# Kernel optimization log

Measured on AMD Instinct MI355X. Metric: run time of the kernel, lower is better.

The kernel has to match this reference:

```python
import jax, jax.numpy as jnp
import numpy as np

N_E = 1024
E_DIM = 256
BETA = 0.25
B, L = 32, 1024


def setup_inputs() -> dict:
    key = jax.random.key(0)
    k1, k2 = jax.random.split(key)
    z = jax.random.normal(k1, (B, E_DIM, L), dtype=jnp.float32)
    mask = jnp.ones((B, L), dtype=jnp.float32)
    embedding = jax.random.uniform(k2, (N_E, E_DIM), dtype=jnp.float32,
                                   minval=-1.0 / N_E, maxval=1.0 / N_E)
    return {"z": z, "mask": mask, "embedding": embedding}


def reference(z, mask, embedding):
    # conv branch: (B, C, L) -> (B, L, C) -> (N, C)
    Bz, C, Lz = z.shape
    zp = jnp.transpose(z, (0, 2, 1))          # (B, L, C)
    zf = zp.reshape(-1, C)                    # (N, C)

    # squared L2 distance to every codebook entry: ||z||^2 + ||e||^2 - 2 z.e
    d = (jnp.sum(zf * zf, axis=1, keepdims=True)
         + jnp.sum(embedding * embedding, axis=1)
         - 2.0 * (zf @ embedding.T))          # (N, n_e)
    idx = jnp.argmin(d, axis=1)               # (N,)

    # gather == one_hot @ embedding
    z_q = embedding[idx].reshape(Bz, Lz, C)   # (B, L, C)

    m = mask[..., None]                       # (B, L, 1)
    commitment_loss = jnp.mean(((jax.lax.stop_gradient(z_q) - zp) * m) ** 2)
    codebook_loss = jnp.mean(((z_q - jax.lax.stop_gradient(zp)) * m) ** 2)
    loss = commitment_loss + BETA * codebook_loss

    # straight-through estimator
    z_q_st = zp + jax.lax.stop_gradient(z_q - zp)

    one_hot = jax.nn.one_hot(idx, N_E, dtype=zf.dtype)           # (N, n_e)
    e_mean = jnp.zeros((N_E,), zf.dtype).at[idx].add(1.0) / idx.shape[0]
    perplexity = jnp.exp(-jnp.sum(e_mean * jnp.log(e_mean + 1e-10)))

    z_q_out = jnp.transpose(z_q_st, (0, 2, 1))  # back to (B, C, L)
    return (loss, z_q_out, perplexity, one_hot, idx[:, None])
```

## Files before the change

### kernel.cpp

```cpp
#include <hip/hip_runtime.h>

constexpr int B_ = 32, C_ = 256, L_ = 1024, NE = 1024;
constexpr int NPTS = B_ * L_;
constexpr long long LOSS_OFF = 0;
constexpr long long ZQ_OFF   = 1;
constexpr long long PERP_OFF = 1 + 8388608;
constexpr long long OH_OFF   = PERP_OFF + 1;
constexpr long long IDX_OFF  = OH_OFF + 33554432LL;
constexpr size_t WS_IDX = 0;
constexpr size_t WS_CNT = 131072;
constexpr size_t WS_LP  = 135168;
constexpr size_t WS_E2  = 139264;

constexpr float MARGIN = 7e-4f;

typedef _Float16 f16x8 __attribute__((ext_vector_type(8)));
typedef float    f32x4 __attribute__((ext_vector_type(4)));

__device__ inline unsigned fkey(float f) {
  unsigned u = __float_as_uint(f);
  return (u & 0x80000000u) ? ~u : (u | 0x80000000u);
}
__device__ inline float unfkey(unsigned k) {
  unsigned u = (k & 0x80000000u) ? (k ^ 0x80000000u) : ~k;
  return __uint_as_float(u);
}

__global__ __launch_bounds__(256) void k_prep_ehl(const float* __restrict__ emb,
                                                  uint4* __restrict__ ehlF) {
  const int u = blockIdx.x * 256 + threadIdx.x;
  const int c16 = u & 15;
  const int s8  = (u >> 4) & 31;
  const int g   = u >> 9;
  const int code = g * 16 + c16;
  const float4* e4 = reinterpret_cast<const float4*>(emb + (size_t)code * C_) + s8 * 2;
  float4 v0 = e4[0], v1 = e4[1];
  const float f[8] = {v0.x, v0.y, v0.z, v0.w, v1.x, v1.y, v1.z, v1.w};
  unsigned w[4];
#pragma unroll
  for (int i = 0; i < 4; ++i) {
    _Float16 h0 = (_Float16)f[2 * i];
    _Float16 h1 = (_Float16)f[2 * i + 1];
    w[i] = (unsigned)__builtin_bit_cast(unsigned short, h0) |
           ((unsigned)__builtin_bit_cast(unsigned short, h1) << 16);
  }
  ehlF[u] = make_uint4(w[0], w[1], w[2], w[3]);
}

__global__ __launch_bounds__(64) void k_prep_e2(const float* __restrict__ emb,
                                                float* __restrict__ e2,
                                                unsigned* __restrict__ counts) {
  const int j = blockIdx.x;
  const int t = threadIdx.x;
  const float* row = emb + (size_t)j * C_;
  double s = 0.0;
#pragma unroll
  for (int q = 0; q < 4; ++q) {
    float v = row[t + 64 * q];
    s += (double)v * (double)v;
  }
#pragma unroll
  for (int off = 32; off > 0; off >>= 1) s += __shfl_down(s, off);
  if (t == 0) { e2[j] = (float)s; counts[j] = 0u; }
}

__global__ __launch_bounds__(512, 1) void k_screen_rr(const float* __restrict__ z,
                                                      const float* __restrict__ emb,
                                                      const uint4* __restrict__ ehlF,
                                                      const float* __restrict__ e2g,
                                                      int* __restrict__ idxw,
                                                      unsigned* __restrict__ counts,
                                                      float* __restrict__ idx_out) {
  __shared__ _Float16 Az[128 * 256];
  __shared__ double zpart[128][17];
  __shared__ unsigned short cand[128 * 32];
  __shared__ unsigned long long bestkey[128];
  __shared__ unsigned minkey[128];
  __shared__ unsigned ccnt[128];
  __shared__ float z2s[128];
  __shared__ int ids[128];
  __shared__ unsigned char dcnt[128];
  __shared__ float zcol[256];
  __shared__ int nbad;

  const int tid  = threadIdx.x;
  const int lane = tid & 63;
  const int wid  = tid >> 6;
  const int wr   = wid >> 2;
  const int wc   = wid & 3;
  const int l15  = lane & 15;
  const int lhi  = lane >> 4;
  const int n0   = blockIdx.x * 128;
  const int b    = blockIdx.x >> 3;
  const int l0   = (blockIdx.x & 7) << 7;

  {
    const float4* z4 = reinterpret_cast<const float4*>(z + (size_t)b * (C_ * L_) + l0);
    const int l4 = tid & 31;
    const int kp = tid >> 5;
    double sj[4] = {0.0, 0.0, 0.0, 0.0};
#pragma unroll
    for (int rr = 0; rr < 8; ++rr) {
      const int k0 = rr * 32 + kp * 2;
      float4 a0 = z4[(size_t)k0 * (L_ / 4) + l4];
      float4 a1 = z4[(size_t)(k0 + 1) * (L_ / 4) + l4];
      const float av0[4] = {a0.x, a0.y, a0.z, a0.w};
      const float av1[4] = {a1.x, a1.y, a1.z, a1.w};
#pragma unroll
      for (int j = 0; j < 4; ++j) {
        _Float16 h0 = (_Float16)av0[j];
        _Float16 h1 = (_Float16)av1[j];
        unsigned pk = (unsigned)__builtin_bit_cast(unsigned short, h0) |
                      ((unsigned)__builtin_bit_cast(unsigned short, h1) << 16);
        const int p = l4 * 4 + j;
        const int slot = k0 >> 3;
        const int addr = p * 256 + ((slot ^ (p & 31)) << 3) + (k0 & 7);
        *reinterpret_cast<unsigned*>(&Az[addr]) = pk;
        sj[j] += (double)av0[j] * (double)av0[j];
        sj[j] += (double)av1[j] * (double)av1[j];
      }
    }
#pragma unroll
    for (int j = 0; j < 4; ++j) zpart[l4 * 4 + j][kp] = sj[j];
  }
  if (tid < 128) { minkey[tid] = 0xFFFFFFFFu; ccnt[tid] = 0u; }
  if (tid == 0) nbad = 0;
  __syncthreads();

  f32x4 acc[4][4];
#pragma unroll
  for (int i = 0; i < 4; ++i)
#pragma unroll
    for (int j = 0; j < 4; ++j) acc[i][j] = (f32x4){0.f, 0.f, 0.f, 0.f};

  for (int ph = 0; ph < 8; ++ph) {
    const int cc = ph >> 1;
    const int kh = ph & 1;
#pragma unroll
    for (int s = 0; s < 4; ++s) {
      const int slotA = kh * 16 + s * 4 + lhi;
      const int slotB = kh * 16 + s * 4 + lhi;
      f16x8 bfr[4];
#pragma unroll
      for (int tj = 0; tj < 4; ++tj) {
        const int g = cc * 16 + wc * 4 + tj;
        bfr[tj] = __builtin_bit_cast(f16x8, ehlF[(g * 32 + slotB) * 16 + l15]);
      }
      f16x8 afr[4];
#pragma unroll
      for (int ti = 0; ti < 4; ++ti) {
        const int pA = wr * 64 + ti * 16 + l15;
        const int swzA = slotA ^ (((ti & 1) << 4) ^ l15);
        afr[ti] = *reinterpret_cast<const f16x8*>(&Az[pA * 256 + swzA * 8]);
      }
#pragma unroll
      for (int ti = 0; ti < 4; ++ti)
#pragma unroll
        for (int tj = 0; tj < 4; ++tj)
          acc[ti][tj] = __builtin_amdgcn_mfma_f32_16x16x32_f16(
              afr[ti], bfr[tj], acc[ti][tj], 0, 0, 0);
    }
    if (kh == 1) {
      float e2r[4];
#pragma unroll
      for (int tj = 0; tj < 4; ++tj)
        e2r[tj] = e2g[cc * 256 + wc * 64 + tj * 16 + l15];
#pragma unroll
      for (int ti = 0; ti < 4; ++ti) {
#pragma unroll
        for (int r = 0; r < 4; ++r) {
          float m = e2r[0] - 2.0f * acc[ti][0][r];
#pragma unroll
          for (int tj = 1; tj < 4; ++tj) {
            float v = e2r[tj] - 2.0f * acc[ti][tj][r];
            m = fminf(m, v);
          }
          m = fminf(m, __shfl_xor(m, 1));
          m = fminf(m, __shfl_xor(m, 2));
          m = fminf(m, __shfl_xor(m, 4));
          m = fminf(m, __shfl_xor(m, 8));
          if (l15 == 0) {
            const int p = wr * 64 + ti * 16 + lhi * 4 + r;
            atomicMin(&minkey[p], fkey(m));
          }
        }
      }
      __syncthreads();
#pragma unroll
      for (int ti = 0; ti < 4; ++ti) {
#pragma unroll
        for (int r = 0; r < 4; ++r) {
          const int p = wr * 64 + ti * 16 + lhi * 4 + r;
          const float thr = unfkey(minkey[p]) + MARGIN;
#pragma unroll
          for (int tj = 0; tj < 4; ++tj) {
            float s = e2r[tj] - 2.0f * acc[ti][tj][r];
            if (s <= thr) {
              unsigned pos = atomicAdd(&ccnt[p], 1u);
              if (pos < 32u)
                cand[p * 32 + pos] = (unsigned short)(cc * 256 + wc * 64 + tj * 16 + l15);
            }
          }
        }
      }
#pragma unroll
      for (int i = 0; i < 4; ++i)
#pragma unroll
        for (int j = 0; j < 4; ++j) acc[i][j] = (f32x4){0.f, 0.f, 0.f, 0.f};
    }
  }
  __syncthreads();

  if (tid < 128) {
    double s = 0.0;
#pragma unroll
    for (int kp = 0; kp < 16; ++kp) s += zpart[tid][kp];
    z2s[tid] = (float)s;
    bestkey[tid] = ~0ULL;
    const unsigned cnt = ccnt[tid];
    if (cnt == 1u) {
      dcnt[tid] = 0;
      ids[tid] = cand[tid * 32];
    } else if (cnt <= 32u) {
      dcnt[tid] = (unsigned char)cnt;
    } else {
      dcnt[tid] = 0xFF;
      atomicAdd(&nbad, 1);
    }
  }
  __syncthreads();

  {
    const int p = tid >> 2, j = tid & 3;
    const int cnt = (dcnt[p] == 0xFF) ? 0 : (int)dcnt[p];
    const float* zc = z + (size_t)b * (C_ * L_) + l0 + p;
    for (int q = j; q < cnt; q += 4) {
      const int c = cand[p * 32 + q];
      const float4* er = reinterpret_cast<const float4*>(emb + (size_t)c * C_);
      float acc2 = 0.f;
#pragma unroll 4
      for (int k4 = 0; k4 < 64; ++k4) {
        float4 e = er[k4];
        acc2 = fmaf(zc[(size_t)(k4 * 4 + 0) * L_], e.x, acc2);
        acc2 = fmaf(zc[(size_t)(k4 * 4 + 1) * L_], e.y, acc2);
        acc2 = fmaf(zc[(size_t)(k4 * 4 + 2) * L_], e.z, acc2);
        acc2 = fmaf(zc[(size_t)(k4 * 4 + 3) * L_], e.w, acc2);
      }
      const float d = (z2s[p] + e2g[c]) - 2.0f * acc2;
      const unsigned long long key =
          ((unsigned long long)fkey(d) << 32) | (unsigned)c;
      atomicMin(&bestkey[p], key);
    }
  }
  __syncthreads();

  if (nbad > 0) {
    for (int p = 0; p < 128; ++p) {
      if (dcnt[p] != 0xFF) continue;
      const float* zc = z + (size_t)b * (C_ * L_) + l0 + p;
      if (tid < 256) zcol[tid] = zc[(size_t)tid * L_];
      __syncthreads();
#pragma unroll
      for (int h = 0; h < 2; ++h) {
        const int c = tid * 2 + h;
        const float* er = emb + (size_t)c * C_;
        float acc2 = 0.f;
        for (int k = 0; k < 256; ++k) acc2 = fmaf(zcol[k], er[k], acc2);
        const float d = (z2s[p] + e2g[c]) - 2.0f * acc2;
        const unsigned long long key =
            ((unsigned long long)fkey(d) << 32) | (unsigned)c;
        atomicMin(&bestkey[p], key);
      }
      __syncthreads();
    }
  }

  if (tid < 128) {
    const int n = n0 + tid;
    int id = ids[tid];
    if (dcnt[tid] != 0) id = (int)(unsigned)(bestkey[tid] & 0xFFFFFFFFu);
    idxw[n] = id;
    idx_out[n] = (float)id;
    atomicAdd(&counts[id], 1u);
  }
}

__global__ __launch_bounds__(256) void k_zq_loss(const float* __restrict__ z,
                                                 const float* __restrict__ emb,
                                                 const float* __restrict__ mask,
                                                 const int* __restrict__ idxw,
                                                 float* __restrict__ zq_out,
                                                 float* __restrict__ lp) {
  __shared__ float eq[256][66];
  __shared__ float red[256];
  const int tid = threadIdx.x, bid = blockIdx.x;
  const int b = bid >> 4, l0 = (bid & 15) << 6, n0 = bid << 6;
  {
    const int r  = tid >> 2;
    const int kq = tid & 3;
    const int id = idxw[n0 + r];
    const float4* e4 = reinterpret_cast<const float4*>(emb + (size_t)id * C_);
#pragma unroll
    for (int rep = 0; rep < 16; ++rep) {
      int c4 = rep * 4 + kq;
      float4 v = e4[c4];
      eq[c4 * 4 + 0][r] = v.x;
      eq[c4 * 4 + 1][r] = v.y;
      eq[c4 * 4 + 2][r] = v.z;
      eq[c4 * 4 + 3][r] = v.w;
    }
  }
  __syncthreads();
  const int lq = tid & 63, cg = tid >> 6;
  const float m = mask[b * L_ + l0 + lq];
  const size_t zbase = (size_t)b * C_ * L_ + l0 + lq;
  float s = 0.f;
#pragma unroll 4
  for (int ci = 0; ci < 64; ++ci) {
    int c = cg * 64 + ci;
    float zv = z[zbase + (size_t)c * L_];
    float q  = eq[c][lq];
    float diff = q - zv;
    zq_out[zbase + (size_t)c * L_] = zv + diff;
    float t = diff * m;
    s = fmaf(t, t, s);
  }
  red[tid] = s;
  __syncthreads();
  for (int off = 128; off > 0; off >>= 1) {
    if (tid < off) red[tid] += red[tid + off];
    __syncthreads();
  }
  if (tid == 0) lp[bid] = red[0];
}

__global__ __launch_bounds__(256) void k_onehot(const int* __restrict__ idxw,
                                                float* __restrict__ oh) {
  const int tid = threadIdx.x, bid = blockIdx.x;
#pragma unroll
  for (int r = 0; r < 16; ++r) {
    const int n = bid * 16 + r;
    const int id = idxw[n];
    float* row = oh + (size_t)n * NE;
    const int c = tid * 4;
    float2 v0, v1;
    v0.x = (c + 0 == id) ? 1.f : 0.f;
    v0.y = (c + 1 == id) ? 1.f : 0.f;
    v1.x = (c + 2 == id) ? 1.f : 0.f;
    v1.y = (c + 3 == id) ? 1.f : 0.f;
    *reinterpret_cast<float2*>(row + c)     = v0;
    *reinterpret_cast<float2*>(row + c + 2) = v1;
  }
}

__global__ __launch_bounds__(256) void k_final(const float* __restrict__ lp,
                                               const unsigned int* __restrict__ counts,
                                               float* __restrict__ out) {
  __shared__ float red[256];
  const int t = threadIdx.x;
  red[t] = lp[t] + lp[t + 256];
  __syncthreads();
  for (int off = 128; off > 0; off >>= 1) {
    if (t < off) red[t] += red[t + off];
    __syncthreads();
  }
  if (t == 0) {
    float m = red[0] / 8388608.0f;
    out[LOSS_OFF] = m + 0.25f * m;
  }
  __syncthreads();
  float h = 0.f;
#pragma unroll
  for (int q = 0; q < 4; ++q) {
    int jj = t * 4 + q;
    float em = (float)counts[jj] * (1.0f / 32768.0f);
    h += em * logf(em + 1e-10f);
  }
  red[t] = h;
  __syncthreads();
  for (int off = 128; off > 0; off >>= 1) {
    if (t < off) red[t] += red[t + off];
    __syncthreads();
  }
  if (t == 0) out[PERP_OFF] = expf(-red[0]);
}

extern "C" void kernel_launch(void* const* d_in, const int* in_sizes, int n_in,
                              void* d_out, int out_size, void* d_ws, size_t ws_size,
                              hipStream_t stream) {
  const float* z    = (const float*)d_in[0];
  const float* mask = (const float*)d_in[1];
  const float* emb  = (const float*)d_in[2];
  float* out = (float*)d_out;
  char* ws = (char*)d_ws;
  int* idxw            = (int*)(ws + WS_IDX);
  unsigned int* counts = (unsigned int*)(ws + WS_CNT);
  float* lp            = (float*)(ws + WS_LP);
  float* e2            = (float*)(ws + WS_E2);

  uintptr_t sp = (uintptr_t)(out + OH_OFF);
  sp = (sp + 15) & ~(uintptr_t)15;
  uint4* ehlF = (uint4*)sp;

  hipLaunchKernelGGL(k_prep_ehl, dim3(128), dim3(256), 0, stream, emb, ehlF);
  hipLaunchKernelGGL(k_prep_e2, dim3(NE), dim3(64), 0, stream, emb, e2, counts);
  hipLaunchKernelGGL(k_screen_rr, dim3(256), dim3(512), 0, stream,
                     z, emb, ehlF, e2, idxw, counts, out + IDX_OFF);
  hipLaunchKernelGGL(k_zq_loss, dim3(512), dim3(256), 0, stream,
                     z, emb, mask, idxw, out + ZQ_OFF, lp);
  hipLaunchKernelGGL(k_onehot, dim3(NPTS / 16), dim3(256), 0, stream,
                     idxw, out + OH_OFF);
  hipLaunchKernelGGL(k_final, dim3(1), dim3(256), 0, stream, lp, counts, out);
}
```

Baseline: 117.6 us.

## Halve accumulator tile and shared memory to fit two blocks per CU

```diff
diff --git a/kernel.cpp b/kernel.cpp
--- a/kernel.cpp
+++ b/kernel.cpp
@@ -64,7 +64,7 @@
   if (t == 0) { e2[j] = (float)s; counts[j] = 0u; }
 }
 
-__global__ __launch_bounds__(512, 1) void k_screen_rr(const float* __restrict__ z,
+__global__ __launch_bounds__(512, 2) void k_screen_rr(const float* __restrict__ z,
                                                       const float* __restrict__ emb,
                                                       const uint4* __restrict__ ehlF,
                                                       const float* __restrict__ e2g,
@@ -72,7 +72,6 @@
                                                       unsigned* __restrict__ counts,
                                                       float* __restrict__ idx_out) {
   __shared__ _Float16 Az[128 * 256];
-  __shared__ double zpart[128][17];
   __shared__ unsigned short cand[128 * 32];
   __shared__ unsigned long long bestkey[128];
   __shared__ unsigned minkey[128];
@@ -98,7 +97,6 @@
     const float4* z4 = reinterpret_cast<const float4*>(z + (size_t)b * (C_ * L_) + l0);
     const int l4 = tid & 31;
     const int kp = tid >> 5;
-    double sj[4] = {0.0, 0.0, 0.0, 0.0};
 #pragma unroll
     for (int rr = 0; rr < 8; ++rr) {
       const int k0 = rr * 32 + kp * 2;
@@ -116,106 +114,109 @@
         const int slot = k0 >> 3;
         const int addr = p * 256 + ((slot ^ (p & 31)) << 3) + (k0 & 7);
         *reinterpret_cast<unsigned*>(&Az[addr]) = pk;
-        sj[j] += (double)av0[j] * (double)av0[j];
-        sj[j] += (double)av1[j] * (double)av1[j];
-      }
-    }
-#pragma unroll
-    for (int j = 0; j < 4; ++j) zpart[l4 * 4 + j][kp] = sj[j];
+      }
+    }
   }
   if (tid < 128) { minkey[tid] = 0xFFFFFFFFu; ccnt[tid] = 0u; }
   if (tid == 0) nbad = 0;
   __syncthreads();
 
-  f32x4 acc[4][4];
+  f32x4 acc[4][2];
 #pragma unroll
   for (int i = 0; i < 4; ++i)
 #pragma unroll
-    for (int j = 0; j < 4; ++j) acc[i][j] = (f32x4){0.f, 0.f, 0.f, 0.f};
-
-  for (int ph = 0; ph < 8; ++ph) {
-    const int cc = ph >> 1;
-    const int kh = ph & 1;
-#pragma unroll
-    for (int s = 0; s < 4; ++s) {
-      const int slotA = kh * 16 + s * 4 + lhi;
-      const int slotB = kh * 16 + s * 4 + lhi;
-      f16x8 bfr[4];
-#pragma unroll
-      for (int tj = 0; tj < 4; ++tj) {
-        const int g = cc * 16 + wc * 4 + tj;
-        bfr[tj] = __builtin_bit_cast(f16x8, ehlF[(g * 32 + slotB) * 16 + l15]);
-      }
-      f16x8 afr[4];
-#pragma unroll
-      for (int ti = 0; ti < 4; ++ti) {
-        const int pA = wr * 64 + ti * 16 + l15;
-        const int swzA = slotA ^ (((ti & 1) << 4) ^ l15);
-        afr[ti] = *reinterpret_cast<const f16x8*>(&Az[pA * 256 + swzA * 8]);
-      }
-#pragma unroll
-      for (int ti = 0; ti < 4; ++ti)
-#pragma unroll
-        for (int tj = 0; tj < 4; ++tj)
-          acc[ti][tj] = __builtin_amdgcn_mfma_f32_16x16x32_f16(
-              afr[ti], bfr[tj], acc[ti][tj], 0, 0, 0);
-    }
-    if (kh == 1) {
-      float e2r[4];
-#pragma unroll
-      for (int tj = 0; tj < 4; ++tj)
-        e2r[tj] = e2g[cc * 256 + wc * 64 + tj * 16 + l15];
-#pragma unroll
-      for (int ti = 0; ti < 4; ++ti) {
-#pragma unroll
-        for (int r = 0; r < 4; ++r) {
-          float m = e2r[0] - 2.0f * acc[ti][0][r];
-#pragma unroll
-          for (int tj = 1; tj < 4; ++tj) {
-            float v = e2r[tj] - 2.0f * acc[ti][tj][r];
-            m = fminf(m, v);
-          }
-          m = fminf(m, __shfl_xor(m, 1));
-          m = fminf(m, __shfl_xor(m, 2));
-          m = fminf(m, __shfl_xor(m, 4));
-          m = fminf(m, __shfl_xor(m, 8));
-          if (l15 == 0) {
-            const int p = wr * 64 + ti * 16 + lhi * 4 + r;
-            atomicMin(&minkey[p], fkey(m));
+    for (int j = 0; j < 2; ++j) acc[i][j] = (f32x4){0.f, 0.f, 0.f, 0.f};
+
+  for (int cc = 0; cc < 8; ++cc) {
+#pragma unroll
+    for (int kh = 0; kh < 2; ++kh) {
+#pragma unroll
+      for (int s = 0; s < 4; ++s) {
+        const int slotA = kh * 16 + s * 4 + lhi;
+        f16x8 bfr[2];
+#pragma unroll
+        for (int tj = 0; tj < 2; ++tj) {
+          const int g = cc * 8 + wc * 2 + tj;
+          bfr[tj] = __builtin_bit_cast(f16x8, ehlF[(g * 32 + slotA) * 16 + l15]);
+        }
+        f16x8 afr[4];
+#pragma unroll
+        for (int ti = 0; ti < 4; ++ti) {
+          const int pA = wr * 64 + ti * 16 + l15;
+          const int swzA = slotA ^ (((ti & 1) << 4) ^ l15);
+          afr[ti] = *reinterpret_cast<const f16x8*>(&Az[pA * 256 + swzA * 8]);
+        }
+#pragma unroll
+        for (int ti = 0; ti < 4; ++ti)
+#pragma unroll
+          for (int tj = 0; tj < 2; ++tj)
+            acc[ti][tj] = __builtin_amdgcn_mfma_f32_16x16x32_f16(
+                afr[ti], bfr[tj], acc[ti][tj], 0, 0, 0);
+      }
+    }
+    float e2r[2];
+#pragma unroll
+    for (int tj = 0; tj < 2; ++tj)
+      e2r[tj] = e2g[cc * 128 + wc * 32 + tj * 16 + l15];
+#pragma unroll
+    for (int ti = 0; ti < 4; ++ti) {
+#pragma unroll
+      for (int r = 0; r < 4; ++r) {
+        float m0 = e2r[0] - 2.0f * acc[ti][0][r];
+        float m1 = e2r[1] - 2.0f * acc[ti][1][r];
+        float m = fminf(m0, m1);
+        m = fminf(m, __shfl_xor(m, 1));
+        m = fminf(m, __shfl_xor(m, 2));
+        m = fminf(m, __shfl_xor(m, 4));
+        m = fminf(m, __shfl_xor(m, 8));
+        if (l15 == 0) {
+          const int p = wr * 64 + ti * 16 + lhi * 4 + r;
+          atomicMin(&minkey[p], fkey(m));
+        }
+      }
+    }
+    __syncthreads();
+#pragma unroll
+    for (int ti = 0; ti < 4; ++ti) {
+#pragma unroll
+      for (int r = 0; r < 4; ++r) {
+        const int p = wr * 64 + ti * 16 + lhi * 4 + r;
+        const float thr = unfkey(minkey[p]) + MARGIN;
+#pragma unroll
+        for (int tj = 0; tj < 2; ++tj) {
+          float s = e2r[tj] - 2.0f * acc[ti][tj][r];
+          if (s <= thr) {
+            unsigned pos = atomicAdd(&ccnt[p], 1u);
+            if (pos < 32u)
+              cand[p * 32 + pos] = (unsigned short)(cc * 128 + wc * 32 + tj * 16 + l15);
           }
         }
       }
-      __syncthreads();
-#pragma unroll
-      for (int ti = 0; ti < 4; ++ti) {
-#pragma unroll
-        for (int r = 0; r < 4; ++r) {
-          const int p = wr * 64 + ti * 16 + lhi * 4 + r;
-          const float thr = unfkey(minkey[p]) + MARGIN;
-#pragma unroll
-          for (int tj = 0; tj < 4; ++tj) {
-            float s = e2r[tj] - 2.0f * acc[ti][tj][r];
-            if (s <= thr) {
-              unsigned pos = atomicAdd(&ccnt[p], 1u);
-              if (pos < 32u)
-                cand[p * 32 + pos] = (unsigned short)(cc * 256 + wc * 64 + tj * 16 + l15);
-            }
-          }
-        }
-      }
-#pragma unroll
-      for (int i = 0; i < 4; ++i)
-#pragma unroll
-        for (int j = 0; j < 4; ++j) acc[i][j] = (f32x4){0.f, 0.f, 0.f, 0.f};
-    }
+    }
+#pragma unroll
+    for (int i = 0; i < 4; ++i)
+#pragma unroll
+      for (int j = 0; j < 2; ++j) acc[i][j] = (f32x4){0.f, 0.f, 0.f, 0.f};
+  }
+  __syncthreads();
+
+  double* zp4 = reinterpret_cast<double*>(Az);
+  {
+    const int p = tid >> 2, j = tid & 3;
+    const float* zc = z + (size_t)b * (C_ * L_) + l0 + p;
+    double s = 0.0;
+#pragma unroll 8
+    for (int k = j * 64; k < j * 64 + 64; ++k) {
+      float v = zc[(size_t)k * L_];
+      s += (double)v * (double)v;
+    }
+    zp4[p * 4 + j] = s;
   }
   __syncthreads();
 
   if (tid < 128) {
-    double s = 0.0;
-#pragma unroll
-    for (int kp = 0; kp < 16; ++kp) s += zpart[tid][kp];
-    z2s[tid] = (float)s;
+    z2s[tid] = (float)(zp4[tid * 4] + zp4[tid * 4 + 1] +
+                       zp4[tid * 4 + 2] + zp4[tid * 4 + 3]);
     bestkey[tid] = ~0ULL;
     const unsigned cnt = ccnt[tid];
     if (cnt == 1u) {
```

After: 148.3 us. 26.2% more time.
